# Kernel optimization log

Hardware: AMD Instinct MI355X
Metric: run time of the kernel (lower is better)

The kernel has to match this reference:

```python
import jax, jax.numpy as jnp
import numpy as np

K = 24            # patch_size (window)
D = 4             # dilation
C = 256           # dim
H = 8             # num_heads
N = 500000        # number of octree tokens at this depth (nnum_t)
BATCH_SIZE = 8
BLOCK = K * D
NA = int(np.ceil(N / BLOCK)) * BLOCK   # nnum_a (padded length)
PAD = NA - N
SCALE = (C // H) ** -0.5
MASK_VAL = -1000.0


def setup_inputs() -> dict:
    key = jax.random.key(0)
    k1, k2, k3, k4 = jax.random.split(key, 4)
    data = jax.random.normal(k1, (N, C), jnp.float32)
    qkv_w = jax.random.normal(k2, (3 * C, C), jnp.float32) * 0.02
    qkv_b = jnp.zeros((3 * C,), jnp.float32)
    proj_w = jax.random.normal(k3, (C, C), jnp.float32) * 0.02
    proj_b = jnp.zeros((C,), jnp.float32)
    batch_idx = jnp.sort(jax.random.randint(k4, (N,), 0, BATCH_SIZE, dtype=jnp.int32))
    return {"data": data, "qkv_w": qkv_w, "qkv_b": qkv_b,
            "proj_w": proj_w, "proj_b": proj_b, "batch_idx": batch_idx}


def _dilate_mask(batch_idx):
    # patch_partition of batch ids: pad with fill_value = batch_size
    b = jnp.concatenate([batch_idx, jnp.full((PAD,), BATCH_SIZE, jnp.int32)], axis=0)
    # dilate reshuffle: (-1, K, D) -> transpose -> (-1, K) windows
    b = b.reshape(-1, K, D).transpose(0, 2, 1).reshape(-1, K)
    diff = b[:, :, None] - b[:, None, :]           # [nw, K, K]
    return jnp.where(diff != 0, MASK_VAL, 0.0).astype(jnp.float32)


def reference(data, qkv_w, qkv_b, proj_w, proj_b, batch_idx):
    mask = _dilate_mask(batch_idx)                              # [nw, K, K]
    # patch_partition of features: pad with zeros
    x = jnp.concatenate([data, jnp.zeros((PAD, C), data.dtype)], axis=0)
    # dilation reshuffle: (-1, K, D, C) -> (-1, D, K, C) -> windows [nw, K, C]
    x = x.reshape(-1, K, D, C).transpose(0, 2, 1, 3).reshape(-1, K, C)
    qkv = (x @ qkv_w.T + qkv_b).reshape(-1, K, 3, H, C // H).transpose(2, 0, 3, 1, 4)
    q, k, v = qkv[0] * SCALE, qkv[1], qkv[2]                    # [nw, H, K, hd]
    attn = jnp.einsum('nhqd,nhkd->nhqk', q, k) + mask[:, None]  # [nw, H, K, K]
    attn = jax.nn.softmax(attn, axis=-1)
    out = jnp.einsum('nhqk,nhkd->nhqd', attn, v)
    out = out.transpose(0, 2, 1, 3).reshape(-1, C)              # merge heads
    # reverse dilation reshuffle, drop padding (patch_reverse)
    out = out.reshape(-1, D, K, C).transpose(0, 2, 1, 3).reshape(-1, C)[:N]
    return out @ proj_w.T + proj_b
```

## Files before the change

### kernel.cpp

```cpp
#include <hip/hip_runtime.h>


#define N_TOK 500000
#define NA    500064
#define MP    500096
#define MT    3907
#define MT8   3912
#define CDIM  256
#define KWIN  24
#define NWIN  20836
#define HEADS 8
#define SCALE_F 0.17677669529663689f

typedef __attribute__((ext_vector_type(8))) short bf16x8;
typedef __attribute__((ext_vector_type(4))) float f32x4;

__device__ __forceinline__ unsigned short f2b(float f) {
    unsigned int u = __float_as_uint(f);
    u += 0x7fffu + ((u >> 16) & 1u);
    return (unsigned short)(u >> 16);
}

#define GLOAD_LDS16(gsrc, ldst) \
    __builtin_amdgcn_global_load_lds((const __attribute__((address_space(1))) void*)(gsrc), \
                                     (__attribute__((address_space(3))) void*)(ldst), 16, 0, 0)


__global__ __launch_bounds__(256) void cvt_w_kernel(const float* __restrict__ src,
                                                    unsigned short* __restrict__ dst, int n8) {
    int i = blockIdx.x * 256 + threadIdx.x;
    if (i >= n8) return;
    float4 a = ((const float4*)src)[i * 2];
    float4 b = ((const float4*)src)[i * 2 + 1];
    uint4 o;
    o.x = (unsigned)f2b(a.x) | ((unsigned)f2b(a.y) << 16);
    o.y = (unsigned)f2b(a.z) | ((unsigned)f2b(a.w) << 16);
    o.z = (unsigned)f2b(b.x) | ((unsigned)f2b(b.y) << 16);
    o.w = (unsigned)f2b(b.z) | ((unsigned)f2b(b.w) << 16);
    ((uint4*)dst)[i] = o;
}

__global__ __launch_bounds__(256) void zero_pad_kernel(unsigned short* __restrict__ dst) {
    int i = blockIdx.x * 256 + threadIdx.x;
    if (i < (MP - N_TOK) * CDIM / 8)
        *(uint4*)(dst + (size_t)N_TOK * CDIM + (size_t)i * 8) = make_uint4(0u, 0u, 0u, 0u);
}


__global__ __launch_bounds__(256, 3) void qkv_gemm_kernel(const float* __restrict__ A32,
                                                          const unsigned short* __restrict__ Bt,
                                                          const float* __restrict__ bias,
                                                          unsigned short* __restrict__ out) {
    __shared__ unsigned short ldsA[128 * 64];
    __shared__ unsigned short ldsB[128 * 64];
    const int l = blockIdx.x;
    const int s = l >> 3;
    const int mtile = (l & 7) + 8 * (s / 6);
    const int ntile = s - (s / 6) * 6;
    if (mtile >= MT) return;

    const int tid  = threadIdx.x;
    const int lane = tid & 63;
    const int wv   = tid >> 6;
    const int wr   = wv >> 1, wc = wv & 1;

    f32x4 acc[4][4];
    #pragma unroll
    for (int i = 0; i < 4; ++i)
        #pragma unroll
        for (int j = 0; j < 4; ++j)
            #pragma unroll
            for (int r = 0; r < 4; ++r) acc[i][j][r] = 0.f;

    const char*  bbase = (const char*)(Bt + (size_t)ntile * 128 * CDIM);
    const int lrow8 = lane >> 3;
    const int lcolb_sw = (((lane & 7) ^ lrow8) << 4);
    const int arow  = tid >> 4;
    const int acol  = (tid & 15) * 4;
    const int awz   = ((tid >> 4) & 7) << 4;
    const int growb = mtile * 128;
    const bool full_tile = (growb + 128 <= N_TOK);
    char* ldsA_b = (char*)ldsA;
    const int lrow = lane & 15, lg = lane >> 4;
    const int swzr = (lrow & 7) << 4;

    for (int kt = 0; kt < 4; ++kt) {
        #pragma unroll
        for (int c = 0; c < 4; ++c) {
            int chunk = wv * 4 + c;
            int row = chunk * 8 + lrow8;
            GLOAD_LDS16(bbase + (size_t)row * 512 + kt * 128 + lcolb_sw, &ldsB[chunk * 512]);
        }
        float4 areg[8];
        if (full_tile) {
            #pragma unroll
            for (int i = 0; i < 8; ++i) {
                int row_g = growb + i * 16 + arow;
                areg[i] = *(const float4*)(A32 + (size_t)row_g * CDIM + kt * 64 + acol);
            }
        } else {
            #pragma unroll
            for (int i = 0; i < 8; ++i) {
                int row_g = growb + i * 16 + arow;
                int row_c = row_g < N_TOK ? row_g : (N_TOK - 1);
                areg[i] = *(const float4*)(A32 + (size_t)row_c * CDIM + kt * 64 + acol);
            }
            #pragma unroll
            for (int i = 0; i < 8; ++i)
                if (growb + i * 16 + arow >= N_TOK) areg[i] = make_float4(0.f, 0.f, 0.f, 0.f);
        }
        #pragma unroll
        for (int i = 0; i < 8; ++i) {
            float4 a = areg[i];
            uint2 o;
            o.x = (unsigned)f2b(a.x) | ((unsigned)f2b(a.y) << 16);
            o.y = (unsigned)f2b(a.z) | ((unsigned)f2b(a.w) << 16);
            *(uint2*)(ldsA_b + (i * 16 + arow) * 128 + (((tid & 15) * 8) ^ awz)) = o;
        }
        __syncthreads();
        #pragma unroll
        for (int ks = 0; ks < 2; ++ks) {
            const int kbyte = ks * 64 + lg * 16;
            bf16x8 af[4], bfr[4];
            #pragma unroll
            for (int i = 0; i < 4; ++i) {
                int ra = wr * 64 + i * 16 + lrow;
                int rb = wc * 64 + i * 16 + lrow;
                af[i]  = *(const bf16x8*)(ldsA_b + ra * 128 + (kbyte ^ swzr));
                bfr[i] = *(const bf16x8*)((const char*)ldsB + rb * 128 + (kbyte ^ swzr));
            }
            #pragma unroll
            for (int i = 0; i < 4; ++i)
                #pragma unroll
                for (int j = 0; j < 4; ++j)
                    acc[i][j] = __builtin_amdgcn_mfma_f32_16x16x32_bf16(af[i], bfr[j], acc[i][j], 0, 0, 0);
        }
        __syncthreads();
    }

    #pragma unroll
    for (int i = 0; i < 4; ++i) {
        int row0 = mtile * 128 + wr * 64 + i * 16 + ((lane >> 4) << 2);
        #pragma unroll
        for (int j = 0; j < 4; ++j) {
            int col = ntile * 128 + wc * 64 + j * 16 + (lane & 15);
            float bv = bias[col];
            #pragma unroll
            for (int r = 0; r < 4; ++r)
                out[(size_t)(row0 + r) * 768 + col] = f2b(acc[i][j][r] + bv);
        }
    }
}


__global__ __launch_bounds__(256, 3) void proj_gemm_kernel(const unsigned short* __restrict__ A,
                                                           const unsigned short* __restrict__ Bt,
                                                           const float* __restrict__ bias,
                                                           float* __restrict__ out) {
    __shared__ unsigned short ldsA[128 * 64];
    __shared__ unsigned short ldsB[128 * 64];
    const int l = blockIdx.x;
    const int s = l >> 3;
    const int mtile = (l & 7) + 8 * (s >> 1);
    const int ntile = s & 1;
    if (mtile >= MT) return;

    const int tid  = threadIdx.x;
    const int lane = tid & 63;
    const int wv   = tid >> 6;
    const int wr   = wv >> 1, wc = wv & 1;

    f32x4 acc[4][4];
    #pragma unroll
    for (int i = 0; i < 4; ++i)
        #pragma unroll
        for (int j = 0; j < 4; ++j)
            #pragma unroll
            for (int r = 0; r < 4; ++r) acc[i][j][r] = 0.f;

    const char* abase = (const char*)(A  + (size_t)mtile * 128 * CDIM);
    const char* bbase = (const char*)(Bt + (size_t)ntile * 128 * CDIM);
    const int lrow8 = lane >> 3;
    const int lcolb_sw = (((lane & 7) ^ lrow8) << 4);
    const int lrow = lane & 15, lg = lane >> 4;
    const int swzr = (lrow & 7) << 4;

    for (int kt = 0; kt < 4; ++kt) {
        const int kb_byte = kt * 128;
        #pragma unroll
        for (int c = 0; c < 4; ++c) {
            int chunk = wv * 4 + c;
            int row = chunk * 8 + lrow8;
            GLOAD_LDS16(abase + (size_t)row * 512 + kb_byte + lcolb_sw, &ldsA[chunk * 512]);
        }
        #pragma unroll
        for (int c = 0; c < 4; ++c) {
            int chunk = wv * 4 + c;
            int row = chunk * 8 + lrow8;
            GLOAD_LDS16(bbase + (size_t)row * 512 + kb_byte + lcolb_sw, &ldsB[chunk * 512]);
        }
        __syncthreads();
        #pragma unroll
        for (int ks = 0; ks < 2; ++ks) {
            const int kbyte = ks * 64 + lg * 16;
            bf16x8 af[4], bfr[4];
            #pragma unroll
            for (int i = 0; i < 4; ++i) {
                int ra = wr * 64 + i * 16 + lrow;
                int rb = wc * 64 + i * 16 + lrow;
                af[i]  = *(const bf16x8*)((const char*)ldsA + ra * 128 + (kbyte ^ swzr));
                bfr[i] = *(const bf16x8*)((const char*)ldsB + rb * 128 + (kbyte ^ swzr));
            }
            #pragma unroll
            for (int i = 0; i < 4; ++i)
                #pragma unroll
                for (int j = 0; j < 4; ++j)
                    acc[i][j] = __builtin_amdgcn_mfma_f32_16x16x32_bf16(af[i], bfr[j], acc[i][j], 0, 0, 0);
        }
        __syncthreads();
    }

    #pragma unroll
    for (int i = 0; i < 4; ++i) {
        int row0 = mtile * 128 + wr * 64 + i * 16 + ((lane >> 4) << 2);
        #pragma unroll
        for (int j = 0; j < 4; ++j) {
            int col = ntile * 128 + wc * 64 + j * 16 + (lane & 15);
            float bv = bias[col];
            #pragma unroll
            for (int r = 0; r < 4; ++r) {
                int row = row0 + r;
                if (row < N_TOK) out[(size_t)row * CDIM + col] = acc[i][j][r] + bv;
            }
        }
    }
}


__global__ __launch_bounds__(256) void attn_kernel(const unsigned short* __restrict__ qkv,
                                                   const int* __restrict__ batch_idx,
                                                   unsigned short* __restrict__ attn_out) {
    __shared__ unsigned short sP[4][32 * 64];
    const int tid  = threadIdx.x;
    const int lane = tid & 63;
    const int ws_  = tid >> 6;
    const int wid  = blockIdx.x * 4 + ws_;
    const int w = wid >> 3, h = wid & 7;
    const int gw = w >> 2, dd = w & 3;
    const int lrow = lane & 15, lg = lane >> 4;
    const int pbase = gw * 96 + dd;

    bf16x8 Qf[2], Kf[2];
    #pragma unroll
    for (int t = 0; t < 2; ++t) {
        size_t p = (size_t)(pbase + (t * 16 + lrow) * 4);
        const unsigned short* bp = qkv + p * 768 + h * 32 + lg * 8;
        Qf[t] = *(const bf16x8*)bp;
        Kf[t] = *(const bf16x8*)(bp + 256);
    }

    unsigned short v0[8], v1[8];
    #pragma unroll
    for (int j2 = 0; j2 < 8; ++j2) {
        size_t p = (size_t)(pbase + (lg * 8 + j2) * 4);
        const unsigned short* vp = qkv + p * 768 + 512 + h * 32 + lrow;
        v0[j2] = vp[0];
        v1[j2] = vp[16];
    }

    int bq[2];
    #pragma unroll
    for (int j = 0; j < 2; ++j) {
        int r = j * 16 + lrow;
        int p = pbase + r * 4;
        bq[j] = (r < KWIN && p < N_TOK) ? batch_idx[p] : -1;
    }
    int bk[2][4];
    #pragma unroll
    for (int i = 0; i < 2; ++i)
        #pragma unroll
        for (int rr = 0; rr < 4; ++rr) {
            int r = i * 16 + lg * 4 + rr;
            int p = pbase + r * 4;
            bk[i][rr] = (r < KWIN && p < N_TOK) ? batch_idx[p] : -2;
        }

    f32x4 accS[2][2];
    #pragma unroll
    for (int i = 0; i < 2; ++i)
        #pragma unroll
        for (int j = 0; j < 2; ++j)
            #pragma unroll
            for (int r = 0; r < 4; ++r) accS[i][j][r] = 0.f;
    #pragma unroll
    for (int i = 0; i < 2; ++i)
        #pragma unroll
        for (int j = 0; j < 2; ++j)
            accS[i][j] = __builtin_amdgcn_mfma_f32_16x16x32_bf16(Kf[i], Qf[j], accS[i][j], 0, 0, 0);

    float sv[2][2][4];
    float mx[2] = { -3.0e38f, -3.0e38f };
    #pragma unroll
    for (int i = 0; i < 2; ++i)
        #pragma unroll
        for (int j = 0; j < 2; ++j)
            #pragma unroll
            for (int rr = 0; rr < 4; ++rr) {
                float val = (bk[i][rr] == bq[j]) ? accS[i][j][rr] * SCALE_F : -1.0e9f;
                sv[i][j][rr] = val;
                mx[j] = fmaxf(mx[j], val);
            }
    mx[0] = fmaxf(mx[0], __shfl_xor(mx[0], 16)); mx[0] = fmaxf(mx[0], __shfl_xor(mx[0], 32));
    mx[1] = fmaxf(mx[1], __shfl_xor(mx[1], 16)); mx[1] = fmaxf(mx[1], __shfl_xor(mx[1], 32));
    float sm[2] = { 0.f, 0.f };
    #pragma unroll
    for (int i = 0; i < 2; ++i)
        #pragma unroll
        for (int j = 0; j < 2; ++j)
            #pragma unroll
            for (int rr = 0; rr < 4; ++rr) {
                float e = __expf(sv[i][j][rr] - mx[j]);
                sv[i][j][rr] = e;
                sm[j] += e;
            }
    sm[0] += __shfl_xor(sm[0], 16); sm[0] += __shfl_xor(sm[0], 32);
    sm[1] += __shfl_xor(sm[1], 16); sm[1] += __shfl_xor(sm[1], 32);
    float inv[2] = { 1.f / sm[0], 1.f / sm[1] };

    char* pb = (char*)sP[ws_];
    const int swz = (lrow & 7) << 4;
    #pragma unroll
    for (int j = 0; j < 2; ++j) {
        int q = j * 16 + lrow;
        #pragma unroll
        for (int i = 0; i < 2; ++i) {
            unsigned lo = (unsigned)f2b(sv[i][j][0] * inv[j]) | ((unsigned)f2b(sv[i][j][1] * inv[j]) << 16);
            unsigned hi = (unsigned)f2b(sv[i][j][2] * inv[j]) | ((unsigned)f2b(sv[i][j][3] * inv[j]) << 16);
            *(uint2*)(pb + q * 128 + ((i * 32 + lg * 8) ^ swz)) = make_uint2(lo, hi);
        }
    }
    bf16x8 AP[2];
    #pragma unroll
    for (int jj = 0; jj < 2; ++jj)
        AP[jj] = *(const bf16x8*)(pb + (jj * 16 + lrow) * 128 + ((lg * 16) ^ swz));

    union { bf16x8 v; unsigned short s[8]; } B0, B1;
    #pragma unroll
    for (int j2 = 0; j2 < 8; ++j2) { B0.s[j2] = v0[j2]; B1.s[j2] = v1[j2]; }
    f32x4 accO[2][2];
    #pragma unroll
    for (int i = 0; i < 2; ++i)
        #pragma unroll
        for (int j = 0; j < 2; ++j)
            #pragma unroll
            for (int r = 0; r < 4; ++r) accO[i][j][r] = 0.f;
    #pragma unroll
    for (int jj = 0; jj < 2; ++jj) {
        accO[jj][0] = __builtin_amdgcn_mfma_f32_16x16x32_bf16(AP[jj], B0.v, accO[jj][0], 0, 0, 0);
        accO[jj][1] = __builtin_amdgcn_mfma_f32_16x16x32_bf16(AP[jj], B1.v, accO[jj][1], 0, 0, 0);
    }

    #pragma unroll
    for (int jj = 0; jj < 2; ++jj)
        #pragma unroll
        for (int rr = 0; rr < 4; ++rr) {
            int q = jj * 16 + lg * 4 + rr;
            int p = pbase + q * 4;
            if (q < KWIN && p < N_TOK) {
                unsigned short* op = attn_out + (size_t)p * CDIM + h * 32;
                op[lrow]      = f2b(accO[jj][0][rr]);
                op[16 + lrow] = f2b(accO[jj][1][rr]);
            }
        }
}


extern "C" void kernel_launch(void* const* d_in, const int* in_sizes, int n_in,
                              void* d_out, int out_size, void* d_ws, size_t ws_size,
                              hipStream_t stream) {
    const float* data    = (const float*)d_in[0];
    const float* qkv_w   = (const float*)d_in[1];
    const float* qkv_b   = (const float*)d_in[2];
    const float* proj_w  = (const float*)d_in[3];
    const float* proj_b  = (const float*)d_in[4];
    const int*   batch_i = (const int*)d_in[5];

    char* ws = (char*)d_ws;
    size_t off = 0;
    unsigned short* qkvB   = (unsigned short*)(ws + off); off += (size_t)MP * 768 * 2;
    unsigned short* attnB  = (unsigned short*)(ws + off); off += (size_t)MP * CDIM * 2;
    unsigned short* wqkvB  = (unsigned short*)(ws + off); off += (size_t)768 * 256 * 2;
    unsigned short* wprojB = (unsigned short*)(ws + off); off += (size_t)256 * 256 * 2;
    if (ws_size < off) return;

    cvt_w_kernel<<<(768 * 256 / 8 + 255) / 256, 256, 0, stream>>>(qkv_w, wqkvB, 768 * 256 / 8);
    cvt_w_kernel<<<(256 * 256 / 8 + 255) / 256, 256, 0, stream>>>(proj_w, wprojB, 256 * 256 / 8);
    zero_pad_kernel<<<12, 256, 0, stream>>>(attnB);

    qkv_gemm_kernel<<<MT8 * 6, 256, 0, stream>>>(data, wqkvB, qkv_b, qkvB);
    attn_kernel<<<NWIN * HEADS / 4, 256, 0, stream>>>(qkvB, batch_i, attnB);
    proj_gemm_kernel<<<MT8 * 2, 256, 0, stream>>>(attnB, wprojB, proj_b, (float*)d_out);
}
```

Baseline: 905.0 us.

## Fuse window attention with output projection in one kernel

Merges the attention kernel and the projection GEMM into a single kernel. Each 512-thread block handles one window with all 8 heads, one wave per head. The per-window attention output is staged in swizzled LDS and multiplied directly by the bf16 projection weights held in registers. This removes the bf16 attention buffer round trip through global memory, the zero-pad kernel and one launch. It also remaps windows across XCDs for locality. In exchange each block reloads a 32-column slice of the projection weights per wave, and the larger blocks with higher register use may lower occupancy.

Measured after the change: 1.005 ms. 1.11x slower.

```diff
diff --git a/kernel.cpp b/kernel.cpp
--- a/kernel.cpp
+++ b/kernel.cpp
@@ -40,12 +40,6 @@
     ((uint4*)dst)[i] = o;
 }
 
-__global__ __launch_bounds__(256) void zero_pad_kernel(unsigned short* __restrict__ dst) {
-    int i = blockIdx.x * 256 + threadIdx.x;
-    if (i < (MP - N_TOK) * CDIM / 8)
-        *(uint4*)(dst + (size_t)N_TOK * CDIM + (size_t)i * 8) = make_uint4(0u, 0u, 0u, 0u);
-}
-
 
 __global__ __launch_bounds__(256, 3) void qkv_gemm_kernel(const float* __restrict__ A32,
                                                           const unsigned short* __restrict__ Bt,
@@ -77,7 +71,7 @@
     const int lcolb_sw = (((lane & 7) ^ lrow8) << 4);
     const int arow  = tid >> 4;
     const int acol  = (tid & 15) * 4;
-    const int awz   = ((tid >> 4) & 7) << 4;
+    const int awz   = (arow & 7) << 4;
     const int growb = mtile * 128;
     const bool full_tile = (growb + 128 <= N_TOK);
     char* ldsA_b = (char*)ldsA;
@@ -140,10 +134,10 @@
 
     #pragma unroll
     for (int i = 0; i < 4; ++i) {
-        int row0 = mtile * 128 + wr * 64 + i * 16 + ((lane >> 4) << 2);
+        int row0 = mtile * 128 + wr * 64 + i * 16 + lg * 4;
         #pragma unroll
         for (int j = 0; j < 4; ++j) {
-            int col = ntile * 128 + wc * 64 + j * 16 + (lane & 15);
+            int col = ntile * 128 + wc * 64 + j * 16 + lrow;
             float bv = bias[col];
             #pragma unroll
             for (int r = 0; r < 4; ++r)
@@ -153,99 +147,22 @@
 }
 
 
-__global__ __launch_bounds__(256, 3) void proj_gemm_kernel(const unsigned short* __restrict__ A,
-                                                           const unsigned short* __restrict__ Bt,
-                                                           const float* __restrict__ bias,
-                                                           float* __restrict__ out) {
-    __shared__ unsigned short ldsA[128 * 64];
-    __shared__ unsigned short ldsB[128 * 64];
-    const int l = blockIdx.x;
-    const int s = l >> 3;
-    const int mtile = (l & 7) + 8 * (s >> 1);
-    const int ntile = s & 1;
-    if (mtile >= MT) return;
+__global__ __launch_bounds__(512, 2) void attn_proj_kernel(const unsigned short* __restrict__ qkv,
+                                                           const int* __restrict__ batch_idx,
+                                                           const unsigned short* __restrict__ wproj,
+                                                           const float* __restrict__ pbias,
+                                                           float* __restrict__ dout) {
+    __shared__ unsigned short sP[8][32 * 64];
+    __shared__ unsigned short sX[32 * 256];
+
+    const int bid = blockIdx.x;
+    const int xcd = bid & 7, sidx = bid >> 3;
+    const int qch = NWIN >> 3, rch = NWIN & 7;
+    const int w = (xcd < rch ? xcd * (qch + 1) : rch * (qch + 1) + (xcd - rch) * qch) + sidx;
 
     const int tid  = threadIdx.x;
     const int lane = tid & 63;
-    const int wv   = tid >> 6;
-    const int wr   = wv >> 1, wc = wv & 1;
-
-    f32x4 acc[4][4];
-    #pragma unroll
-    for (int i = 0; i < 4; ++i)
-        #pragma unroll
-        for (int j = 0; j < 4; ++j)
-            #pragma unroll
-            for (int r = 0; r < 4; ++r) acc[i][j][r] = 0.f;
-
-    const char* abase = (const char*)(A  + (size_t)mtile * 128 * CDIM);
-    const char* bbase = (const char*)(Bt + (size_t)ntile * 128 * CDIM);
-    const int lrow8 = lane >> 3;
-    const int lcolb_sw = (((lane & 7) ^ lrow8) << 4);
-    const int lrow = lane & 15, lg = lane >> 4;
-    const int swzr = (lrow & 7) << 4;
-
-    for (int kt = 0; kt < 4; ++kt) {
-        const int kb_byte = kt * 128;
-        #pragma unroll
-        for (int c = 0; c < 4; ++c) {
-            int chunk = wv * 4 + c;
-            int row = chunk * 8 + lrow8;
-            GLOAD_LDS16(abase + (size_t)row * 512 + kb_byte + lcolb_sw, &ldsA[chunk * 512]);
-        }
-        #pragma unroll
-        for (int c = 0; c < 4; ++c) {
-            int chunk = wv * 4 + c;
-            int row = chunk * 8 + lrow8;
-            GLOAD_LDS16(bbase + (size_t)row * 512 + kb_byte + lcolb_sw, &ldsB[chunk * 512]);
-        }
-        __syncthreads();
-        #pragma unroll
-        for (int ks = 0; ks < 2; ++ks) {
-            const int kbyte = ks * 64 + lg * 16;
-            bf16x8 af[4], bfr[4];
-            #pragma unroll
-            for (int i = 0; i < 4; ++i) {
-                int ra = wr * 64 + i * 16 + lrow;
-                int rb = wc * 64 + i * 16 + lrow;
-                af[i]  = *(const bf16x8*)((const char*)ldsA + ra * 128 + (kbyte ^ swzr));
-                bfr[i] = *(const bf16x8*)((const char*)ldsB + rb * 128 + (kbyte ^ swzr));
-            }
-            #pragma unroll
-            for (int i = 0; i < 4; ++i)
-                #pragma unroll
-                for (int j = 0; j < 4; ++j)
-                    acc[i][j] = __builtin_amdgcn_mfma_f32_16x16x32_bf16(af[i], bfr[j], acc[i][j], 0, 0, 0);
-        }
-        __syncthreads();
-    }
-
-    #pragma unroll
-    for (int i = 0; i < 4; ++i) {
-        int row0 = mtile * 128 + wr * 64 + i * 16 + ((lane >> 4) << 2);
-        #pragma unroll
-        for (int j = 0; j < 4; ++j) {
-            int col = ntile * 128 + wc * 64 + j * 16 + (lane & 15);
-            float bv = bias[col];
-            #pragma unroll
-            for (int r = 0; r < 4; ++r) {
-                int row = row0 + r;
-                if (row < N_TOK) out[(size_t)row * CDIM + col] = acc[i][j][r] + bv;
-            }
-        }
-    }
-}
-
-
-__global__ __launch_bounds__(256) void attn_kernel(const unsigned short* __restrict__ qkv,
-                                                   const int* __restrict__ batch_idx,
-                                                   unsigned short* __restrict__ attn_out) {
-    __shared__ unsigned short sP[4][32 * 64];
-    const int tid  = threadIdx.x;
-    const int lane = tid & 63;
-    const int ws_  = tid >> 6;
-    const int wid  = blockIdx.x * 4 + ws_;
-    const int w = wid >> 3, h = wid & 7;
+    const int h    = tid >> 6;
     const int gw = w >> 2, dd = w & 3;
     const int lrow = lane & 15, lg = lane >> 4;
     const int pbase = gw * 96 + dd;
@@ -258,7 +175,6 @@
         Qf[t] = *(const bf16x8*)bp;
         Kf[t] = *(const bf16x8*)(bp + 256);
     }
-
     unsigned short v0[8], v1[8];
     #pragma unroll
     for (int j2 = 0; j2 < 8; ++j2) {
@@ -267,7 +183,6 @@
         v0[j2] = vp[0];
         v1[j2] = vp[16];
     }
-
     int bq[2];
     #pragma unroll
     for (int j = 0; j < 2; ++j) {
@@ -327,7 +242,7 @@
     sm[1] += __shfl_xor(sm[1], 16); sm[1] += __shfl_xor(sm[1], 32);
     float inv[2] = { 1.f / sm[0], 1.f / sm[1] };
 
-    char* pb = (char*)sP[ws_];
+    char* pb = (char*)sP[h];
     const int swz = (lrow & 7) << 4;
     #pragma unroll
     for (int j = 0; j < 2; ++j) {
@@ -360,18 +275,61 @@
         accO[jj][1] = __builtin_amdgcn_mfma_f32_16x16x32_bf16(AP[jj], B1.v, accO[jj][1], 0, 0, 0);
     }
 
+    char* xb = (char*)sX;
     #pragma unroll
     for (int jj = 0; jj < 2; ++jj)
         #pragma unroll
-        for (int rr = 0; rr < 4; ++rr) {
-            int q = jj * 16 + lg * 4 + rr;
-            int p = pbase + q * 4;
-            if (q < KWIN && p < N_TOK) {
-                unsigned short* op = attn_out + (size_t)p * CDIM + h * 32;
-                op[lrow]      = f2b(accO[jj][0][rr]);
-                op[16 + lrow] = f2b(accO[jj][1][rr]);
-            }
-        }
+        for (int nd = 0; nd < 2; ++nd)
+            #pragma unroll
+            for (int rr = 0; rr < 4; ++rr) {
+                int q = jj * 16 + lg * 4 + rr;
+                int c = h * 32 + nd * 16 + lrow;
+                *(unsigned short*)(xb + q * 512 + ((c * 2) ^ ((q & 15) << 4))) = f2b(accO[jj][nd][rr]);
+            }
+
+    bf16x8 WB[2][8];
+    #pragma unroll
+    for (int nt = 0; nt < 2; ++nt)
+        #pragma unroll
+        for (int k8 = 0; k8 < 8; ++k8)
+            WB[nt][k8] = *(const bf16x8*)(wproj + (size_t)(h * 32 + nt * 16 + lrow) * 256 + k8 * 32 + lg * 8);
+
+    __syncthreads();
+
+    f32x4 acc2[2][2];
+    #pragma unroll
+    for (int mt = 0; mt < 2; ++mt)
+        #pragma unroll
+        for (int nt = 0; nt < 2; ++nt)
+            #pragma unroll
+            for (int r = 0; r < 4; ++r) acc2[mt][nt][r] = 0.f;
+    #pragma unroll
+    for (int k8 = 0; k8 < 8; ++k8) {
+        bf16x8 aA[2];
+        #pragma unroll
+        for (int mt = 0; mt < 2; ++mt)
+            aA[mt] = *(const bf16x8*)(xb + (mt * 16 + lrow) * 512 + ((k8 * 64 + lg * 16) ^ (lrow << 4)));
+        #pragma unroll
+        for (int mt = 0; mt < 2; ++mt)
+            #pragma unroll
+            for (int nt = 0; nt < 2; ++nt)
+                acc2[mt][nt] = __builtin_amdgcn_mfma_f32_16x16x32_bf16(aA[mt], WB[nt][k8], acc2[mt][nt], 0, 0, 0);
+    }
+
+    #pragma unroll
+    for (int nt = 0; nt < 2; ++nt) {
+        int n = h * 32 + nt * 16 + lrow;
+        float bv = pbias[n];
+        #pragma unroll
+        for (int mt = 0; mt < 2; ++mt)
+            #pragma unroll
+            for (int rr = 0; rr < 4; ++rr) {
+                int q = mt * 16 + lg * 4 + rr;
+                int p = pbase + q * 4;
+                if (q < KWIN && p < N_TOK)
+                    dout[(size_t)p * CDIM + n] = acc2[mt][nt][rr] + bv;
+            }
+    }
 }
 
 
@@ -388,16 +346,13 @@
     char* ws = (char*)d_ws;
     size_t off = 0;
     unsigned short* qkvB   = (unsigned short*)(ws + off); off += (size_t)MP * 768 * 2;
-    unsigned short* attnB  = (unsigned short*)(ws + off); off += (size_t)MP * CDIM * 2;
     unsigned short* wqkvB  = (unsigned short*)(ws + off); off += (size_t)768 * 256 * 2;
     unsigned short* wprojB = (unsigned short*)(ws + off); off += (size_t)256 * 256 * 2;
     if (ws_size < off) return;
 
     cvt_w_kernel<<<(768 * 256 / 8 + 255) / 256, 256, 0, stream>>>(qkv_w, wqkvB, 768 * 256 / 8);
     cvt_w_kernel<<<(256 * 256 / 8 + 255) / 256, 256, 0, stream>>>(proj_w, wprojB, 256 * 256 / 8);
-    zero_pad_kernel<<<12, 256, 0, stream>>>(attnB);
 
     qkv_gemm_kernel<<<MT8 * 6, 256, 0, stream>>>(data, wqkvB, qkv_b, qkvB);
-    attn_kernel<<<NWIN * HEADS / 4, 256, 0, stream>>>(qkvB, batch_i, attnB);
-    proj_gemm_kernel<<<MT8 * 2, 256, 0, stream>>>(attnB, wprojB, proj_b, (float*)d_out);
-}
+    attn_proj_kernel<<<NWIN, 512, 0, stream>>>(qkvB, batch_i, wprojB, proj_b, (float*)d_out);
+}
```

## Enlarge GEMM tiles to 256x128 with 512-thread blocks

Applied to the files above, without the earlier changes.

Both the QKV and projection GEMMs now use 256-row M tiles computed by 8 waves per block instead of 128-row tiles with 4 waves, so each loaded weight tile is reused across twice as many rows. LDS staging, grid sizes, padding constants and workspace sizes are scaled to match. The intent is to cut redundant B-tile traffic and per-block overhead, at the cost of more LDS per block, fewer resident blocks, and a coarser tail tile.

Measured after the change: 930.8 us. +2.9%, slower.

```diff
diff --git a/kernel.cpp b/kernel.cpp
--- a/kernel.cpp
+++ b/kernel.cpp
@@ -3,9 +3,8 @@
 
 #define N_TOK 500000
 #define NA    500064
-#define MP    500096
-#define MT    3907
-#define MT8   3912
+#define MP2   500224
+#define MT2   1954
 #define CDIM  256
 #define KWIN  24
 #define NWIN  20836
@@ -42,22 +41,22 @@
 
 __global__ __launch_bounds__(256) void zero_pad_kernel(unsigned short* __restrict__ dst) {
     int i = blockIdx.x * 256 + threadIdx.x;
-    if (i < (MP - N_TOK) * CDIM / 8)
+    if (i < (MP2 - N_TOK) * CDIM / 8)
         *(uint4*)(dst + (size_t)N_TOK * CDIM + (size_t)i * 8) = make_uint4(0u, 0u, 0u, 0u);
 }
 
 
-__global__ __launch_bounds__(256, 3) void qkv_gemm_kernel(const float* __restrict__ A32,
+__global__ __launch_bounds__(512, 4) void qkv_gemm_kernel(const float* __restrict__ A32,
                                                           const unsigned short* __restrict__ Bt,
                                                           const float* __restrict__ bias,
                                                           unsigned short* __restrict__ out) {
-    __shared__ unsigned short ldsA[128 * 64];
+    __shared__ unsigned short ldsA[256 * 64];
     __shared__ unsigned short ldsB[128 * 64];
     const int l = blockIdx.x;
     const int s = l >> 3;
     const int mtile = (l & 7) + 8 * (s / 6);
     const int ntile = s - (s / 6) * 6;
-    if (mtile >= MT) return;
+    if (mtile >= MT2) return;
 
     const int tid  = threadIdx.x;
     const int lane = tid & 63;
@@ -77,17 +76,17 @@
     const int lcolb_sw = (((lane & 7) ^ lrow8) << 4);
     const int arow  = tid >> 4;
     const int acol  = (tid & 15) * 4;
-    const int awz   = ((tid >> 4) & 7) << 4;
-    const int growb = mtile * 128;
-    const bool full_tile = (growb + 128 <= N_TOK);
+    const int awz   = (arow & 7) << 4;
+    const int growb = mtile * 256;
+    const bool full_tile = (growb + 256 <= N_TOK);
     char* ldsA_b = (char*)ldsA;
     const int lrow = lane & 15, lg = lane >> 4;
     const int swzr = (lrow & 7) << 4;
 
     for (int kt = 0; kt < 4; ++kt) {
         #pragma unroll
-        for (int c = 0; c < 4; ++c) {
-            int chunk = wv * 4 + c;
+        for (int c = 0; c < 2; ++c) {
+            int chunk = c * 8 + wv;
             int row = chunk * 8 + lrow8;
             GLOAD_LDS16(bbase + (size_t)row * 512 + kt * 128 + lcolb_sw, &ldsB[chunk * 512]);
         }
@@ -95,19 +94,19 @@
         if (full_tile) {
             #pragma unroll
             for (int i = 0; i < 8; ++i) {
-                int row_g = growb + i * 16 + arow;
+                int row_g = growb + i * 32 + arow;
                 areg[i] = *(const float4*)(A32 + (size_t)row_g * CDIM + kt * 64 + acol);
             }
         } else {
             #pragma unroll
             for (int i = 0; i < 8; ++i) {
-                int row_g = growb + i * 16 + arow;
+                int row_g = growb + i * 32 + arow;
                 int row_c = row_g < N_TOK ? row_g : (N_TOK - 1);
                 areg[i] = *(const float4*)(A32 + (size_t)row_c * CDIM + kt * 64 + acol);
             }
             #pragma unroll
             for (int i = 0; i < 8; ++i)
-                if (growb + i * 16 + arow >= N_TOK) areg[i] = make_float4(0.f, 0.f, 0.f, 0.f);
+                if (growb + i * 32 + arow >= N_TOK) areg[i] = make_float4(0.f, 0.f, 0.f, 0.f);
         }
         #pragma unroll
         for (int i = 0; i < 8; ++i) {
@@ -115,7 +114,7 @@
             uint2 o;
             o.x = (unsigned)f2b(a.x) | ((unsigned)f2b(a.y) << 16);
             o.y = (unsigned)f2b(a.z) | ((unsigned)f2b(a.w) << 16);
-            *(uint2*)(ldsA_b + (i * 16 + arow) * 128 + (((tid & 15) * 8) ^ awz)) = o;
+            *(uint2*)(ldsA_b + (i * 32 + arow) * 128 + (((tid & 15) * 8) ^ awz)) = o;
         }
         __syncthreads();
         #pragma unroll
@@ -140,10 +139,10 @@
 
     #pragma unroll
     for (int i = 0; i < 4; ++i) {
-        int row0 = mtile * 128 + wr * 64 + i * 16 + ((lane >> 4) << 2);
+        int row0 = mtile * 256 + wr * 64 + i * 16 + lg * 4;
         #pragma unroll
         for (int j = 0; j < 4; ++j) {
-            int col = ntile * 128 + wc * 64 + j * 16 + (lane & 15);
+            int col = ntile * 128 + wc * 64 + j * 16 + lrow;
             float bv = bias[col];
             #pragma unroll
             for (int r = 0; r < 4; ++r)
@@ -153,17 +152,17 @@
 }
 
 
-__global__ __launch_bounds__(256, 3) void proj_gemm_kernel(const unsigned short* __restrict__ A,
+__global__ __launch_bounds__(512, 4) void proj_gemm_kernel(const unsigned short* __restrict__ A,
                                                            const unsigned short* __restrict__ Bt,
                                                            const float* __restrict__ bias,
                                                            float* __restrict__ out) {
-    __shared__ unsigned short ldsA[128 * 64];
+    __shared__ unsigned short ldsA[256 * 64];
     __shared__ unsigned short ldsB[128 * 64];
     const int l = blockIdx.x;
     const int s = l >> 3;
     const int mtile = (l & 7) + 8 * (s >> 1);
     const int ntile = s & 1;
-    if (mtile >= MT) return;
+    if (mtile >= MT2) return;
 
     const int tid  = threadIdx.x;
     const int lane = tid & 63;
@@ -178,7 +177,7 @@
             #pragma unroll
             for (int r = 0; r < 4; ++r) acc[i][j][r] = 0.f;
 
-    const char* abase = (const char*)(A  + (size_t)mtile * 128 * CDIM);
+    const char* abase = (const char*)(A  + (size_t)mtile * 256 * CDIM);
     const char* bbase = (const char*)(Bt + (size_t)ntile * 128 * CDIM);
     const int lrow8 = lane >> 3;
     const int lcolb_sw = (((lane & 7) ^ lrow8) << 4);
@@ -186,18 +185,17 @@
     const int swzr = (lrow & 7) << 4;
 
     for (int kt = 0; kt < 4; ++kt) {
-        const int kb_byte = kt * 128;
         #pragma unroll
         for (int c = 0; c < 4; ++c) {
-            int chunk = wv * 4 + c;
+            int chunk = c * 8 + wv;
             int row = chunk * 8 + lrow8;
-            GLOAD_LDS16(abase + (size_t)row * 512 + kb_byte + lcolb_sw, &ldsA[chunk * 512]);
-        }
-        #pragma unroll
-        for (int c = 0; c < 4; ++c) {
-            int chunk = wv * 4 + c;
+            GLOAD_LDS16(abase + (size_t)row * 512 + kt * 128 + lcolb_sw, &ldsA[chunk * 512]);
+        }
+        #pragma unroll
+        for (int c = 0; c < 2; ++c) {
+            int chunk = c * 8 + wv;
             int row = chunk * 8 + lrow8;
-            GLOAD_LDS16(bbase + (size_t)row * 512 + kb_byte + lcolb_sw, &ldsB[chunk * 512]);
+            GLOAD_LDS16(bbase + (size_t)row * 512 + kt * 128 + lcolb_sw, &ldsB[chunk * 512]);
         }
         __syncthreads();
         #pragma unroll
@@ -222,10 +220,10 @@
 
     #pragma unroll
     for (int i = 0; i < 4; ++i) {
-        int row0 = mtile * 128 + wr * 64 + i * 16 + ((lane >> 4) << 2);
+        int row0 = mtile * 256 + wr * 64 + i * 16 + lg * 4;
         #pragma unroll
         for (int j = 0; j < 4; ++j) {
-            int col = ntile * 128 + wc * 64 + j * 16 + (lane & 15);
+            int col = ntile * 128 + wc * 64 + j * 16 + lrow;
             float bv = bias[col];
             #pragma unroll
             for (int r = 0; r < 4; ++r) {
@@ -387,17 +385,17 @@
 
     char* ws = (char*)d_ws;
     size_t off = 0;
-    unsigned short* qkvB   = (unsigned short*)(ws + off); off += (size_t)MP * 768 * 2;
-    unsigned short* attnB  = (unsigned short*)(ws + off); off += (size_t)MP * CDIM * 2;
+    unsigned short* qkvB   = (unsigned short*)(ws + off); off += (size_t)MP2 * 768 * 2;
+    unsigned short* attnB  = (unsigned short*)(ws + off); off += (size_t)MP2 * CDIM * 2;
     unsigned short* wqkvB  = (unsigned short*)(ws + off); off += (size_t)768 * 256 * 2;
     unsigned short* wprojB = (unsigned short*)(ws + off); off += (size_t)256 * 256 * 2;
     if (ws_size < off) return;
 
     cvt_w_kernel<<<(768 * 256 / 8 + 255) / 256, 256, 0, stream>>>(qkv_w, wqkvB, 768 * 256 / 8);
     cvt_w_kernel<<<(256 * 256 / 8 + 255) / 256, 256, 0, stream>>>(proj_w, wprojB, 256 * 256 / 8);
-    zero_pad_kernel<<<12, 256, 0, stream>>>(attnB);
-
-    qkv_gemm_kernel<<<MT8 * 6, 256, 0, stream>>>(data, wqkvB, qkv_b, qkvB);
+    zero_pad_kernel<<<28, 256, 0, stream>>>(attnB);
+
+    qkv_gemm_kernel<<<8 * 6 * 245, 512, 0, stream>>>(data, wqkvB, qkv_b, qkvB);
     attn_kernel<<<NWIN * HEADS / 4, 256, 0, stream>>>(qkvB, batch_i, attnB);
-    proj_gemm_kernel<<<MT8 * 2, 256, 0, stream>>>(attnB, wprojB, proj_b, (float*)d_out);
-}
+    proj_gemm_kernel<<<8 * 2 * 245, 512, 0, stream>>>(attnB, wprojB, proj_b, (float*)d_out);
+}
```

## Store QKV in dilated-window order so attention reads contiguous rows

Applied to the files above, without the earlier changes.

The QKV GEMM epilogue now scatters each output row into its dilated-window slot, so every attention window occupies 24 consecutive rows instead of rows strided by 4. The attention kernel writes its output in that same window order, and the projection GEMM epilogue undoes the permutation when it stores the final rows. The intent is to replace strided, poorly coalesced Q/K/V gathers in attention with contiguous row reads. Attention blocks are also remapped with an interleaving swizzle, and the zero-padding kernel is dropped because padded rows are never stored. The cost is scattered row stores and integer division in both GEMM epilogues, and rows in the padded tail are left uninitialised.

After: 950.7 us. +5.1%, slower.

```diff
diff --git a/kernel.cpp b/kernel.cpp
--- a/kernel.cpp
+++ b/kernel.cpp
@@ -40,12 +40,6 @@
     ((uint4*)dst)[i] = o;
 }
 
-__global__ __launch_bounds__(256) void zero_pad_kernel(unsigned short* __restrict__ dst) {
-    int i = blockIdx.x * 256 + threadIdx.x;
-    if (i < (MP - N_TOK) * CDIM / 8)
-        *(uint4*)(dst + (size_t)N_TOK * CDIM + (size_t)i * 8) = make_uint4(0u, 0u, 0u, 0u);
-}
-
 
 __global__ __launch_bounds__(256, 3) void qkv_gemm_kernel(const float* __restrict__ A32,
                                                           const unsigned short* __restrict__ Bt,
@@ -77,7 +71,7 @@
     const int lcolb_sw = (((lane & 7) ^ lrow8) << 4);
     const int arow  = tid >> 4;
     const int acol  = (tid & 15) * 4;
-    const int awz   = ((tid >> 4) & 7) << 4;
+    const int awz   = (arow & 7) << 4;
     const int growb = mtile * 128;
     const bool full_tile = (growb + 128 <= N_TOK);
     char* ldsA_b = (char*)ldsA;
@@ -140,14 +134,24 @@
 
     #pragma unroll
     for (int i = 0; i < 4; ++i) {
-        int row0 = mtile * 128 + wr * 64 + i * 16 + ((lane >> 4) << 2);
+        int row0 = mtile * 128 + wr * 64 + i * 16 + lg * 4;
         #pragma unroll
         for (int j = 0; j < 4; ++j) {
-            int col = ntile * 128 + wc * 64 + j * 16 + (lane & 15);
+            int col = ntile * 128 + wc * 64 + j * 16 + lrow;
             float bv = bias[col];
             #pragma unroll
-            for (int r = 0; r < 4; ++r)
-                out[(size_t)(row0 + r) * 768 + col] = f2b(acc[i][j][r] + bv);
+            for (int r = 0; r < 4; ++r) {
+                int p = row0 + r;
+                int slot;
+                if (p < NA) {
+                    int g  = p / 96;
+                    int rr = p - g * 96;
+                    slot = g * 96 + (rr & 3) * 24 + (rr >> 2);
+                } else {
+                    slot = p;
+                }
+                out[(size_t)slot * 768 + col] = f2b(acc[i][j][r] + bv);
+            }
         }
     }
 }
@@ -222,15 +226,23 @@
 
     #pragma unroll
     for (int i = 0; i < 4; ++i) {
-        int row0 = mtile * 128 + wr * 64 + i * 16 + ((lane >> 4) << 2);
+        int row0 = mtile * 128 + wr * 64 + i * 16 + lg * 4;
         #pragma unroll
         for (int j = 0; j < 4; ++j) {
-            int col = ntile * 128 + wc * 64 + j * 16 + (lane & 15);
+            int col = ntile * 128 + wc * 64 + j * 16 + lrow;
             float bv = bias[col];
             #pragma unroll
             for (int r = 0; r < 4; ++r) {
-                int row = row0 + r;
-                if (row < N_TOK) out[(size_t)row * CDIM + col] = acc[i][j][r] + bv;
+                int pr = row0 + r;
+                if (pr < NA) {
+                    int g  = pr / 96;
+                    int rr = pr - g * 96;
+                    int dd = rr / 24;
+                    int k  = rr - dd * 24;
+                    int p  = g * 96 + k * 4 + dd;
+                    if (p < N_TOK)
+                        out[(size_t)p * CDIM + col] = acc[i][j][r] + bv;
+                }
             }
         }
     }
@@ -241,20 +253,24 @@
                                                    const int* __restrict__ batch_idx,
                                                    unsigned short* __restrict__ attn_out) {
     __shared__ unsigned short sP[4][32 * 64];
+    const int pb = blockIdx.x;
+    const int lb = (pb & 7) * 5209 + (pb >> 3);
     const int tid  = threadIdx.x;
     const int lane = tid & 63;
     const int ws_  = tid >> 6;
-    const int wid  = blockIdx.x * 4 + ws_;
+    const int wid  = lb * 4 + ws_;
     const int w = wid >> 3, h = wid & 7;
     const int gw = w >> 2, dd = w & 3;
     const int lrow = lane & 15, lg = lane >> 4;
-    const int pbase = gw * 96 + dd;
+    const int wbase = gw * 96 + dd * 24;
+    const int obase = gw * 96 + dd;
 
     bf16x8 Qf[2], Kf[2];
     #pragma unroll
     for (int t = 0; t < 2; ++t) {
-        size_t p = (size_t)(pbase + (t * 16 + lrow) * 4);
-        const unsigned short* bp = qkv + p * 768 + h * 32 + lg * 8;
+        int q  = t * 16 + lrow;
+        int sr = wbase + (q < KWIN ? q : 0);
+        const unsigned short* bp = qkv + (size_t)sr * 768 + h * 32 + lg * 8;
         Qf[t] = *(const bf16x8*)bp;
         Kf[t] = *(const bf16x8*)(bp + 256);
     }
@@ -262,8 +278,9 @@
     unsigned short v0[8], v1[8];
     #pragma unroll
     for (int j2 = 0; j2 < 8; ++j2) {
-        size_t p = (size_t)(pbase + (lg * 8 + j2) * 4);
-        const unsigned short* vp = qkv + p * 768 + 512 + h * 32 + lrow;
+        int k  = lg * 8 + j2;
+        int sr = wbase + (k < KWIN ? k : 0);
+        const unsigned short* vp = qkv + (size_t)sr * 768 + 512 + h * 32 + lrow;
         v0[j2] = vp[0];
         v1[j2] = vp[16];
     }
@@ -271,18 +288,18 @@
     int bq[2];
     #pragma unroll
     for (int j = 0; j < 2; ++j) {
-        int r = j * 16 + lrow;
-        int p = pbase + r * 4;
-        bq[j] = (r < KWIN && p < N_TOK) ? batch_idx[p] : -1;
+        int q = j * 16 + lrow;
+        int p = obase + q * 4;
+        bq[j] = (q < KWIN && p < N_TOK) ? batch_idx[p] : -1;
     }
     int bk[2][4];
     #pragma unroll
     for (int i = 0; i < 2; ++i)
         #pragma unroll
         for (int rr = 0; rr < 4; ++rr) {
-            int r = i * 16 + lg * 4 + rr;
-            int p = pbase + r * 4;
-            bk[i][rr] = (r < KWIN && p < N_TOK) ? batch_idx[p] : -2;
+            int k = i * 16 + lg * 4 + rr;
+            int p = obase + k * 4;
+            bk[i][rr] = (k < KWIN && p < N_TOK) ? batch_idx[p] : -2;
         }
 
     f32x4 accS[2][2];
@@ -327,7 +344,7 @@
     sm[1] += __shfl_xor(sm[1], 16); sm[1] += __shfl_xor(sm[1], 32);
     float inv[2] = { 1.f / sm[0], 1.f / sm[1] };
 
-    char* pb = (char*)sP[ws_];
+    char* pb_ = (char*)sP[ws_];
     const int swz = (lrow & 7) << 4;
     #pragma unroll
     for (int j = 0; j < 2; ++j) {
@@ -336,13 +353,13 @@
         for (int i = 0; i < 2; ++i) {
             unsigned lo = (unsigned)f2b(sv[i][j][0] * inv[j]) | ((unsigned)f2b(sv[i][j][1] * inv[j]) << 16);
             unsigned hi = (unsigned)f2b(sv[i][j][2] * inv[j]) | ((unsigned)f2b(sv[i][j][3] * inv[j]) << 16);
-            *(uint2*)(pb + q * 128 + ((i * 32 + lg * 8) ^ swz)) = make_uint2(lo, hi);
+            *(uint2*)(pb_ + q * 128 + ((i * 32 + lg * 8) ^ swz)) = make_uint2(lo, hi);
         }
     }
     bf16x8 AP[2];
     #pragma unroll
     for (int jj = 0; jj < 2; ++jj)
-        AP[jj] = *(const bf16x8*)(pb + (jj * 16 + lrow) * 128 + ((lg * 16) ^ swz));
+        AP[jj] = *(const bf16x8*)(pb_ + (jj * 16 + lrow) * 128 + ((lg * 16) ^ swz));
 
     union { bf16x8 v; unsigned short s[8]; } B0, B1;
     #pragma unroll
@@ -365,9 +382,9 @@
         #pragma unroll
         for (int rr = 0; rr < 4; ++rr) {
             int q = jj * 16 + lg * 4 + rr;
-            int p = pbase + q * 4;
+            int p = obase + q * 4;
             if (q < KWIN && p < N_TOK) {
-                unsigned short* op = attn_out + (size_t)p * CDIM + h * 32;
+                unsigned short* op = attn_out + (size_t)(wbase + q) * CDIM + h * 32;
                 op[lrow]      = f2b(accO[jj][0][rr]);
                 op[16 + lrow] = f2b(accO[jj][1][rr]);
             }
@@ -395,9 +412,8 @@
 
     cvt_w_kernel<<<(768 * 256 / 8 + 255) / 256, 256, 0, stream>>>(qkv_w, wqkvB, 768 * 256 / 8);
     cvt_w_kernel<<<(256 * 256 / 8 + 255) / 256, 256, 0, stream>>>(proj_w, wprojB, 256 * 256 / 8);
-    zero_pad_kernel<<<12, 256, 0, stream>>>(attnB);
 
     qkv_gemm_kernel<<<MT8 * 6, 256, 0, stream>>>(data, wqkvB, qkv_b, qkvB);
-    attn_kernel<<<NWIN * HEADS / 4, 256, 0, stream>>>(qkvB, batch_i, attnB);
+    attn_kernel<<<NWIN * 2, 256, 0, stream>>>(qkvB, batch_i, attnB);
     proj_gemm_kernel<<<MT8 * 2, 256, 0, stream>>>(attnB, wprojB, proj_b, (float*)d_out);
 }
```
